# Kernel tuning notes

Measured on AMD Instinct MI355X. Metric: run time of the kernel, lower is better.

Reference implementation:

```python
import jax, jax.numpy as jnp
import numpy as np

B, L, D, H = 2, 4096, 512, 8
DK = D // H


def setup_inputs() -> dict:
    key = jax.random.key(0)
    ks = jax.random.split(key, 12)
    s = 1.0 / np.sqrt(D)
    inp = {
        "q": jax.random.normal(ks[0], (B, L, D), jnp.float32),
        "k": jax.random.normal(ks[1], (B, L, D), jnp.float32),
        "v": jax.random.normal(ks[2], (B, L, D), jnp.float32),
        # causal mask, broadcast over batch and heads: [1,1,Lq,Lk]
        "mask": jnp.tril(jnp.ones((L, L), jnp.int32))[None, None],
        "Wq": jax.random.normal(ks[3], (D, D), jnp.float32) * s,
        "bq": jnp.zeros((D,), jnp.float32),
        "Wk": jax.random.normal(ks[4], (D, D), jnp.float32) * s,
        "bk": jnp.zeros((D,), jnp.float32),
        "Wv": jax.random.normal(ks[5], (D, D), jnp.float32) * s,
        "bv": jnp.zeros((D,), jnp.float32),
        "Wo": jax.random.normal(ks[6], (D, D), jnp.float32) * s,
        "bo": jnp.zeros((D,), jnp.float32),
    }
    return inp


def reference(q, k, v, mask, Wq, bq, Wk, bk, Wv, bv, Wo, bo):
    # Linear projections (torch Linear: x @ W.T + b); here W stored as [D_in, D_out]
    def split_heads(x):  # [B,L,D] -> [B,H,L,dk]
        return x.reshape(B, L, H, DK).transpose(0, 2, 1, 3)

    qh = split_heads(q @ Wq + bq)
    kh = split_heads(k @ Wk + bk)
    vh = split_heads(v @ Wv + bv)

    scale = 1.0 / np.sqrt(DK).astype(np.float32)
    scores = jnp.einsum("bhqd,bhkd->bhqk", qh, kh) * scale  # [B,H,Lq,Lk]
    scores = jnp.where(mask == 0, jnp.float32(-jnp.inf), scores)
    attn = jax.nn.softmax(scores, axis=-1)
    # dropout is identity in eval mode
    ctx = jnp.einsum("bhqk,bhkd->bhqd", attn, vh)  # [B,H,Lq,dk]
    ctx = ctx.transpose(0, 2, 1, 3).reshape(B, L, D)
    return ctx @ Wo + bo
```

## Files before the change

kernel.cpp:

```cpp
#include <hip/hip_runtime.h>
#include <hip/hip_bf16.h>
#include <math.h>

#define BB 2
#define LL 4096
#define DD 512
#define HH 8
#define DKK 64

typedef short bf16x8 __attribute__((ext_vector_type(8)));
typedef float f32x4 __attribute__((ext_vector_type(4)));

__device__ __forceinline__ unsigned short f2bf(float x) {
    __hip_bfloat16 h = __float2bfloat16(x);
    return *reinterpret_cast<unsigned short*>(&h);
}

__device__ __forceinline__ int swzi64(int row, int byte) {
    return row * 64 + ((byte ^ ((row & 7) << 4)) >> 1);
}

__global__ __launch_bounds__(256) void wt_kernel(
    const float* __restrict__ W0, const float* __restrict__ W1,
    const float* __restrict__ W2, const float* __restrict__ W3,
    unsigned short* __restrict__ Wt)
{
    __shared__ unsigned short T[64][72];
    const int tid = threadIdx.x;
    const int n0 = blockIdx.x * 64, k0 = blockIdx.y * 64, mz = blockIdx.z;
    const float* W = (mz == 0) ? W0 : (mz == 1) ? W1 : (mz == 2) ? W2 : W3;
    unsigned short* out = Wt + (size_t)mz * DD * DD;

#pragma unroll
    for (int it = 0; it < 2; ++it) {
        int f = tid + it * 256;
        int row = f >> 3, c8 = f & 7;
        const float* src = &W[(size_t)(k0 + row) * DD + n0 + c8 * 8];
        float4 a = *(const float4*)src, b = *(const float4*)(src + 4);
        T[c8 * 8 + 0][row] = f2bf(a.x); T[c8 * 8 + 1][row] = f2bf(a.y);
        T[c8 * 8 + 2][row] = f2bf(a.z); T[c8 * 8 + 3][row] = f2bf(a.w);
        T[c8 * 8 + 4][row] = f2bf(b.x); T[c8 * 8 + 5][row] = f2bf(b.y);
        T[c8 * 8 + 6][row] = f2bf(b.z); T[c8 * 8 + 7][row] = f2bf(b.w);
    }
    __syncthreads();
    const int d = tid >> 2, c = tid & 3;
    uint4 w0 = *(const uint4*)&T[d][c * 16];
    uint4 w1 = *(const uint4*)&T[d][c * 16 + 8];
    unsigned short* dst = &out[(size_t)(n0 + d) * DD + k0 + c * 16];
    *(uint4*)dst = w0;
    *(uint4*)(dst + 8) = w1;
}

__global__ __launch_bounds__(256) void proj_mfma(
    const float* __restrict__ X, const unsigned short* __restrict__ Wt,
    const float* __restrict__ bias, float* __restrict__ Yf,
    unsigned short* __restrict__ Ybf, int mode)
{
    __shared__ unsigned short Al[64 * 64];
    __shared__ unsigned short Bl[64 * 64];

    const int tid  = threadIdx.x;
    const int wave = tid >> 6;
    const int lane = tid & 63;
    const int lg   = lane >> 4;
    const int lc   = lane & 15;
    const int m0 = blockIdx.x * 64, n0 = blockIdx.y * 64;

    const f32x4 vzero = {0.f, 0.f, 0.f, 0.f};
    f32x4 acc[4] = {vzero, vzero, vzero, vzero};

    for (int kt = 0; kt < 8; ++kt) {
        __syncthreads();
#pragma unroll
        for (int it = 0; it < 2; ++it) {
            int f = tid + it * 256;
            int row = f >> 3, c8 = f & 7;
            const float* src = &X[(size_t)(m0 + row) * DD + kt * 64 + c8 * 8];
            float4 a = *(const float4*)src, b = *(const float4*)(src + 4);
            unsigned short h[8] = {f2bf(a.x), f2bf(a.y), f2bf(a.z), f2bf(a.w),
                                   f2bf(b.x), f2bf(b.y), f2bf(b.z), f2bf(b.w)};
            *(uint4*)&Al[swzi64(row, c8 * 16)] = *(const uint4*)h;
            const unsigned short* wsrc =
                &Wt[(size_t)(n0 + row) * DD + kt * 64 + c8 * 8];
            *(uint4*)&Bl[swzi64(row, c8 * 16)] = *(const uint4*)wsrc;
        }
        __syncthreads();

#pragma unroll
        for (int kc = 0; kc < 2; ++kc) {
            bf16x8 af = *(const bf16x8*)&Al[swzi64(wave * 16 + lc, kc * 64 + lg * 16)];
#pragma unroll
            for (int nt = 0; nt < 4; ++nt) {
                bf16x8 bf = *(const bf16x8*)&Bl[swzi64(nt * 16 + lc, kc * 64 + lg * 16)];
                acc[nt] = __builtin_amdgcn_mfma_f32_16x16x32_bf16(af, bf, acc[nt], 0, 0, 0);
            }
        }
    }

    float bv[4];
#pragma unroll
    for (int nt = 0; nt < 4; ++nt) bv[nt] = bias[n0 + nt * 16 + lc];

    if (mode == 0) {
#pragma unroll
        for (int nt = 0; nt < 4; ++nt)
#pragma unroll
            for (int r = 0; r < 4; ++r)
                Yf[(size_t)(m0 + wave * 16 + lg * 4 + r) * DD + n0 + nt * 16 + lc] =
                    acc[nt][r] + bv[nt];
    } else if (mode == 1) {
        const int h = n0 >> 6;
        const int b_ = m0 >> 12;
        const int lb = m0 & (LL - 1);
#pragma unroll
        for (int nt = 0; nt < 4; ++nt)
#pragma unroll
            for (int r = 0; r < 4; ++r) {
                int l_ = lb + wave * 16 + lg * 4 + r;
                Ybf[(((size_t)b_ * HH + h) * LL + l_) * DKK + nt * 16 + lc] =
                    f2bf(acc[nt][r] + bv[nt]);
            }
    } else {
        __syncthreads();
#pragma unroll
        for (int nt = 0; nt < 4; ++nt)
#pragma unroll
            for (int r = 0; r < 4; ++r)
                Al[swzi64(nt * 16 + lc, (wave * 16 + lg * 4 + r) * 2)] =
                    f2bf(acc[nt][r] + bv[nt]);
        __syncthreads();
        const int h = n0 >> 6, b_ = m0 >> 12, l0 = m0 & (LL - 1);
        const int d = tid >> 2, c = tid & 3;
        uint4 w0 = *(const uint4*)&Al[swzi64(d, c * 32)];
        uint4 w1 = *(const uint4*)&Al[swzi64(d, c * 32 + 16)];
        unsigned short* dst = &Ybf[(((size_t)b_ * HH + h) * DKK + d) * LL + l0 + c * 16];
        *(uint4*)dst = w0;
        *(uint4*)(dst + 8) = w1;
    }
}

__global__ __launch_bounds__(256) void flash_mfma(
    const unsigned short* __restrict__ qh, const unsigned short* __restrict__ kh,
    const unsigned short* __restrict__ vt, float* __restrict__ ctx)
{
    __shared__ unsigned short Kl[64 * 64];
    __shared__ unsigned short Vl[64 * 64];
    __shared__ unsigned short Pl[64 * 64];

    const int tid  = threadIdx.x;
    const int wave = tid >> 6;
    const int lane = tid & 63;
    const int lg   = lane >> 4;
    const int lc   = lane & 15;
    const int bh   = blockIdx.x;
    const int qt   = (int)gridDim.y - 1 - (int)blockIdx.y;

    const size_t bhoff = (size_t)bh * (LL * DKK);
    const unsigned short* qb = qh + bhoff;
    const unsigned short* kb = kh + bhoff;
    const unsigned short* vb = vt + bhoff;

    auto swzi = [](int row, int byte) {
        return row * 64 + ((byte ^ ((row & 7) << 4)) >> 1);
    };

    const int qrow = qt * 64 + wave * 16 + lc;
    const bf16x8 qf0 = *(const bf16x8*)&qb[(size_t)qrow * DKK + 0 * 32 + lg * 8];
    const bf16x8 qf1 = *(const bf16x8*)&qb[(size_t)qrow * DKK + 1 * 32 + lg * 8];

    const f32x4 vzero = {0.f, 0.f, 0.f, 0.f};
    f32x4 O[4] = {vzero, vzero, vzero, vzero};
    float m_[4] = {-1e30f, -1e30f, -1e30f, -1e30f};
    float l_[4] = {0.f, 0.f, 0.f, 0.f};
    const float scale = 0.125f;

    const int srow = tid >> 2;
    const int sc   = tid & 3;

    for (int kt = 0; kt <= qt; ++kt) {
        __syncthreads();
        {
            const unsigned short* gk = &kb[(size_t)(kt * 64 + srow) * DKK + sc * 16];
            uint4 k0 = *(const uint4*)gk;
            uint4 k1 = *(const uint4*)(gk + 8);
            const unsigned short* gv = &vb[(size_t)srow * LL + kt * 64 + sc * 16];
            uint4 v0 = *(const uint4*)gv;
            uint4 v1 = *(const uint4*)(gv + 8);
            *(uint4*)&Kl[swzi(srow, sc * 32)]      = k0;
            *(uint4*)&Kl[swzi(srow, sc * 32 + 16)] = k1;
            *(uint4*)&Vl[swzi(srow, sc * 32)]      = v0;
            *(uint4*)&Vl[swzi(srow, sc * 32 + 16)] = v1;
        }
        __syncthreads();

        f32x4 s[4];
#pragma unroll
        for (int ct = 0; ct < 4; ++ct) {
            bf16x8 kf0 = *(const bf16x8*)&Kl[swzi(16 * ct + lc, 0 * 64 + 16 * lg)];
            bf16x8 kf1 = *(const bf16x8*)&Kl[swzi(16 * ct + lc, 1 * 64 + 16 * lg)];
            f32x4 a = vzero;
            a = __builtin_amdgcn_mfma_f32_16x16x32_bf16(qf0, kf0, a, 0, 0, 0);
            a = __builtin_amdgcn_mfma_f32_16x16x32_bf16(qf1, kf1, a, 0, 0, 0);
            s[ct] = a;
        }

#pragma unroll
        for (int ct = 0; ct < 4; ++ct)
#pragma unroll
            for (int r = 0; r < 4; ++r)
                s[ct][r] *= scale;
        if (kt == qt) {
#pragma unroll
            for (int ct = 0; ct < 4; ++ct) {
                int kv = 16 * ct + lc;
#pragma unroll
                for (int r = 0; r < 4; ++r)
                    if (kv > wave * 16 + lg * 4 + r) s[ct][r] = -1e30f;
            }
        }

        float rmax[4], rsum[4];
#pragma unroll
        for (int r = 0; r < 4; ++r) {
            float v = fmaxf(fmaxf(s[0][r], s[1][r]), fmaxf(s[2][r], s[3][r]));
            v = fmaxf(v, __shfl_xor(v, 1));
            v = fmaxf(v, __shfl_xor(v, 2));
            v = fmaxf(v, __shfl_xor(v, 4));
            v = fmaxf(v, __shfl_xor(v, 8));
            rmax[r] = v;
        }

#pragma unroll
        for (int r = 0; r < 4; ++r) {
            float mn = fmaxf(m_[r], rmax[r]);
            float f  = __expf(m_[r] - mn);
            m_[r] = mn;
            float rs = 0.f;
#pragma unroll
            for (int ct = 0; ct < 4; ++ct) {
                float p = __expf(s[ct][r] - mn);
                s[ct][r] = p;
                rs += p;
            }
            rsum[r] = rs;
            l_[r] *= f;
#pragma unroll
            for (int dt = 0; dt < 4; ++dt) O[dt][r] *= f;
        }
#pragma unroll
        for (int r = 0; r < 4; ++r) {
            float v = rsum[r];
            v += __shfl_xor(v, 1);
            v += __shfl_xor(v, 2);
            v += __shfl_xor(v, 4);
            v += __shfl_xor(v, 8);
            l_[r] += v;
        }

#pragma unroll
        for (int r = 0; r < 4; ++r) {
            int row = wave * 16 + lg * 4 + r;
#pragma unroll
            for (int ct = 0; ct < 4; ++ct)
                Pl[swzi(row, 32 * ct + 2 * lc)] = f2bf(s[ct][r]);
        }

        bf16x8 pa0 = *(const bf16x8*)&Pl[swzi(wave * 16 + lc, 0 * 64 + 16 * lg)];
        bf16x8 pa1 = *(const bf16x8*)&Pl[swzi(wave * 16 + lc, 1 * 64 + 16 * lg)];
#pragma unroll
        for (int dt = 0; dt < 4; ++dt) {
            bf16x8 vf0 = *(const bf16x8*)&Vl[swzi(16 * dt + lc, 0 * 64 + 16 * lg)];
            bf16x8 vf1 = *(const bf16x8*)&Vl[swzi(16 * dt + lc, 1 * 64 + 16 * lg)];
            O[dt] = __builtin_amdgcn_mfma_f32_16x16x32_bf16(pa0, vf0, O[dt], 0, 0, 0);
            O[dt] = __builtin_amdgcn_mfma_f32_16x16x32_bf16(pa1, vf1, O[dt], 0, 0, 0);
        }
    }

    const int b_ = bh >> 3;
    const int h_ = bh & 7;
#pragma unroll
    for (int r = 0; r < 4; ++r) {
        float inv = 1.0f / l_[r];
        int q = qt * 64 + wave * 16 + lg * 4 + r;
        float* cp = &ctx[((size_t)b_ * LL + q) * DD + h_ * DKK + lc];
#pragma unroll
        for (int dt = 0; dt < 4; ++dt)
            cp[16 * dt] = O[dt][r] * inv;
    }
}

extern "C" void kernel_launch(void* const* d_in, const int* in_sizes, int n_in,
                              void* d_out, int out_size, void* d_ws, size_t ws_size,
                              hipStream_t stream) {
    const float* q  = (const float*)d_in[0];
    const float* k  = (const float*)d_in[1];
    const float* v  = (const float*)d_in[2];
    const float* Wq = (const float*)d_in[4];
    const float* bq = (const float*)d_in[5];
    const float* Wk = (const float*)d_in[6];
    const float* bk = (const float*)d_in[7];
    const float* Wv = (const float*)d_in[8];
    const float* bv = (const float*)d_in[9];
    const float* Wo = (const float*)d_in[10];
    const float* bo = (const float*)d_in[11];
    float* out = (float*)d_out;

    const size_t nBH = (size_t)BB * HH * LL * DKK;
    unsigned short* qh_bf = (unsigned short*)d_ws;
    unsigned short* kh_bf = qh_bf + nBH;
    unsigned short* vt_bf = kh_bf + nBH;
    float* ctx = (float*)(vt_bf + nBH);
    unsigned short* wt4 = (unsigned short*)(ctx + nBH);

    unsigned short* wtq = wt4;
    unsigned short* wtk = wt4 + (size_t)DD * DD;
    unsigned short* wtv = wt4 + (size_t)2 * DD * DD;
    unsigned short* wto = wt4 + (size_t)3 * DD * DD;

    wt_kernel<<<dim3(8, 8, 4), 256, 0, stream>>>(Wq, Wk, Wv, Wo, wt4);

    dim3 pg(128, 8), pb(256);
    proj_mfma<<<pg, pb, 0, stream>>>(q, wtq, bq, nullptr, qh_bf, 1);
    proj_mfma<<<pg, pb, 0, stream>>>(k, wtk, bk, nullptr, kh_bf, 1);
    proj_mfma<<<pg, pb, 0, stream>>>(v, wtv, bv, nullptr, vt_bf, 2);

    flash_mfma<<<dim3(16, 64), 256, 0, stream>>>(qh_bf, kh_bf, vt_bf, ctx);

    proj_mfma<<<pg, pb, 0, stream>>>(ctx, wto, bo, out, nullptr, 0);
}
```

Before: 324.6 us.

## Pre-convert projection inputs to pre-swizzled bf16 tiles before GEMM

```diff
diff --git a/kernel.cpp b/kernel.cpp
--- a/kernel.cpp
+++ b/kernel.cpp
@@ -18,6 +18,26 @@
 
 __device__ __forceinline__ int swzi64(int row, int byte) {
     return row * 64 + ((byte ^ ((row & 7) << 4)) >> 1);
+}
+
+__global__ __launch_bounds__(256) void cvt_tile(
+    const float* __restrict__ X, unsigned short* __restrict__ out)
+{
+    const int tid = threadIdx.x;
+    const int mt = blockIdx.x, kt = blockIdx.y;
+    const int row = tid >> 2, c = tid & 3;
+    const float* src = &X[(size_t)(mt * 64 + row) * DD + kt * 64 + c * 16];
+    float4 a = *(const float4*)src;
+    float4 b = *(const float4*)(src + 4);
+    float4 e = *(const float4*)(src + 8);
+    float4 g = *(const float4*)(src + 12);
+    unsigned short h0[8] = {f2bf(a.x), f2bf(a.y), f2bf(a.z), f2bf(a.w),
+                            f2bf(b.x), f2bf(b.y), f2bf(b.z), f2bf(b.w)};
+    unsigned short h1[8] = {f2bf(e.x), f2bf(e.y), f2bf(e.z), f2bf(e.w),
+                            f2bf(g.x), f2bf(g.y), f2bf(g.z), f2bf(g.w)};
+    unsigned short* t = out + ((size_t)mt * 8 + kt) * 4096;
+    *(uint4*)&t[swzi64(row, c * 32)]      = *(const uint4*)h0;
+    *(uint4*)&t[swzi64(row, c * 32 + 16)] = *(const uint4*)h1;
 }
 
 __global__ __launch_bounds__(256) void wt_kernel(
@@ -46,13 +66,13 @@
     const int d = tid >> 2, c = tid & 3;
     uint4 w0 = *(const uint4*)&T[d][c * 16];
     uint4 w1 = *(const uint4*)&T[d][c * 16 + 8];
-    unsigned short* dst = &out[(size_t)(n0 + d) * DD + k0 + c * 16];
-    *(uint4*)dst = w0;
-    *(uint4*)(dst + 8) = w1;
+    unsigned short* t = out + ((size_t)blockIdx.x * 8 + blockIdx.y) * 4096;
+    *(uint4*)&t[swzi64(d, c * 32)]      = w0;
+    *(uint4*)&t[swzi64(d, c * 32 + 16)] = w1;
 }
 
 __global__ __launch_bounds__(256) void proj_mfma(
-    const float* __restrict__ X, const unsigned short* __restrict__ Wt,
+    const unsigned short* __restrict__ Xt, const unsigned short* __restrict__ Wt,
     const float* __restrict__ bias, float* __restrict__ Yf,
     unsigned short* __restrict__ Ybf, int mode)
 {
@@ -66,23 +86,25 @@
     const int lc   = lane & 15;
     const int m0 = blockIdx.x * 64, n0 = blockIdx.y * 64;
 
+    const unsigned short* Abase = Xt + (size_t)(m0 >> 6) * 8 * 4096;
+    const unsigned short* Bbase = Wt + (size_t)(n0 >> 6) * 8 * 4096;
+
     const f32x4 vzero = {0.f, 0.f, 0.f, 0.f};
     f32x4 acc[4] = {vzero, vzero, vzero, vzero};
 
     for (int kt = 0; kt < 8; ++kt) {
         __syncthreads();
-#pragma unroll
-        for (int it = 0; it < 2; ++it) {
-            int f = tid + it * 256;
-            int row = f >> 3, c8 = f & 7;
-            const float* src = &X[(size_t)(m0 + row) * DD + kt * 64 + c8 * 8];
-            float4 a = *(const float4*)src, b = *(const float4*)(src + 4);
-            unsigned short h[8] = {f2bf(a.x), f2bf(a.y), f2bf(a.z), f2bf(a.w),
-                                   f2bf(b.x), f2bf(b.y), f2bf(b.z), f2bf(b.w)};
-            *(uint4*)&Al[swzi64(row, c8 * 16)] = *(const uint4*)h;
-            const unsigned short* wsrc =
-                &Wt[(size_t)(n0 + row) * DD + kt * 64 + c8 * 8];
-            *(uint4*)&Bl[swzi64(row, c8 * 16)] = *(const uint4*)wsrc;
+        {
+            const unsigned short* At = Abase + kt * 4096;
+            const unsigned short* Bt = Bbase + kt * 4096;
+            uint4 a0 = *(const uint4*)&At[tid * 8];
+            uint4 a1 = *(const uint4*)&At[2048 + tid * 8];
+            uint4 b0 = *(const uint4*)&Bt[tid * 8];
+            uint4 b1 = *(const uint4*)&Bt[2048 + tid * 8];
+            *(uint4*)&Al[tid * 8]        = a0;
+            *(uint4*)&Al[2048 + tid * 8] = a1;
+            *(uint4*)&Bl[tid * 8]        = b0;
+            *(uint4*)&Bl[2048 + tid * 8] = b1;
         }
         __syncthreads();
 
@@ -311,6 +333,7 @@
     unsigned short* vt_bf = kh_bf + nBH;
     float* ctx = (float*)(vt_bf + nBH);
     unsigned short* wt4 = (unsigned short*)(ctx + nBH);
+    unsigned short* xbf = wt4 + (size_t)4 * DD * DD;
 
     unsigned short* wtq = wt4;
     unsigned short* wtk = wt4 + (size_t)DD * DD;
@@ -319,12 +342,16 @@
 
     wt_kernel<<<dim3(8, 8, 4), 256, 0, stream>>>(Wq, Wk, Wv, Wo, wt4);
 
-    dim3 pg(128, 8), pb(256);
-    proj_mfma<<<pg, pb, 0, stream>>>(q, wtq, bq, nullptr, qh_bf, 1);
-    proj_mfma<<<pg, pb, 0, stream>>>(k, wtk, bk, nullptr, kh_bf, 1);
-    proj_mfma<<<pg, pb, 0, stream>>>(v, wtv, bv, nullptr, vt_bf, 2);
+    dim3 cg(128, 8), pg(128, 8), pb(256);
+    cvt_tile<<<cg, pb, 0, stream>>>(q, xbf);
+    proj_mfma<<<pg, pb, 0, stream>>>(xbf, wtq, bq, nullptr, qh_bf, 1);
+    cvt_tile<<<cg, pb, 0, stream>>>(k, xbf);
+    proj_mfma<<<pg, pb, 0, stream>>>(xbf, wtk, bk, nullptr, kh_bf, 1);
+    cvt_tile<<<cg, pb, 0, stream>>>(v, xbf);
+    proj_mfma<<<pg, pb, 0, stream>>>(xbf, wtv, bv, nullptr, vt_bf, 2);
 
     flash_mfma<<<dim3(16, 64), 256, 0, stream>>>(qh_bf, kh_bf, vt_bf, ctx);
 
-    proj_mfma<<<pg, pb, 0, stream>>>(ctx, wto, bo, out, nullptr, 0);
-}
+    cvt_tile<<<cg, pb, 0, stream>>>(ctx, xbf);
+    proj_mfma<<<pg, pb, 0, stream>>>(xbf, wto, bo, out, nullptr, 0);
+}
```

Measured after the change: 321.0 us. About the same (-1.1%).
